# Kernel optimization log

Measured on AMD Instinct MI355X. Metric: run time of the kernel, lower is better.

Reference implementation:

```python
import jax, jax.numpy as jnp
import numpy as np

IN_DIM = 128
HID = 512


def _cell(x, h, c, Wih, Whh, bih, bhh):
    # PyTorch LSTMCell: gates = x @ Wih^T + bih + h @ Whh^T + bhh, order i,f,g,o
    g = x @ Wih.T + h @ Whh.T + (bih + bhh)
    i, f, gg, o = jnp.split(g, 4, axis=-1)
    c2 = jax.nn.sigmoid(f) * c + jax.nn.sigmoid(i) * jnp.tanh(gg)
    h2 = jax.nn.sigmoid(o) * jnp.tanh(c2)
    return h2, c2


def setup_inputs() -> dict:
    key = jax.random.key(0)
    ks = jax.random.split(key, 12)
    s1 = 1.0 / np.sqrt(HID)  # torch LSTMCell init scale
    so = 1.0 / np.sqrt(HID)
    inp = {
        "x": jax.random.normal(ks[0], (128, 1024, IN_DIM), dtype=jnp.float32),
        "Wih1": jax.random.uniform(ks[1], (4 * HID, IN_DIM), jnp.float32, -s1, s1),
        "Whh1": jax.random.uniform(ks[2], (4 * HID, HID), jnp.float32, -s1, s1),
        "bih1": jax.random.uniform(ks[3], (4 * HID,), jnp.float32, -s1, s1),
        "bhh1": jax.random.uniform(ks[4], (4 * HID,), jnp.float32, -s1, s1),
        "Wih_r": jax.random.uniform(ks[5], (4, 4 * HID, HID), jnp.float32, -s1, s1),
        "Whh_r": jax.random.uniform(ks[6], (4, 4 * HID, HID), jnp.float32, -s1, s1),
        "bih_r": jax.random.uniform(ks[7], (4, 4 * HID), jnp.float32, -s1, s1),
        "bhh_r": jax.random.uniform(ks[8], (4, 4 * HID), jnp.float32, -s1, s1),
        "Wout": jax.random.uniform(ks[9], (IN_DIM, HID), jnp.float32, -so, so),
        "bout": jax.random.uniform(ks[10], (IN_DIM,), jnp.float32, -so, so),
        "future": 0,
    }
    return inp


def reference(x, Wih1, Whh1, bih1, bhh1, Wih_r, Whh_r, bih_r, bhh_r, Wout, bout, future):
    B, T, D = x.shape
    z = jnp.zeros((B, HID), dtype=x.dtype)
    carry0 = tuple(z for _ in range(10))  # (h1,c1,...,h5,c5)

    def stack_step(carry, xt):
        h1, c1, h2, c2, h3, c3, h4, c4, h5, c5 = carry
        h1, c1 = _cell(xt, h1, c1, Wih1, Whh1, bih1, bhh1)
        h2, c2 = _cell(h1, h2, c2, Wih_r[0], Whh_r[0], bih_r[0], bhh_r[0])
        h3, c3 = _cell(h2, h3, c3, Wih_r[1], Whh_r[1], bih_r[1], bhh_r[1])
        h4, c4 = _cell(h3, h4, c4, Wih_r[2], Whh_r[2], bih_r[2], bhh_r[2])
        h5, c5 = _cell(h4, h5, c5, Wih_r[3], Whh_r[3], bih_r[3], bhh_r[3])
        return (h1, c1, h2, c2, h3, c3, h4, c4, h5, c5), h5

    carry, h5_seq = jax.lax.scan(stack_step, carry0, jnp.swapaxes(x, 0, 1))  # [T,B,H]
    outputs = jnp.einsum('tbh,dh->tbd', h5_seq, Wout) + bout  # [T,B,D]
    outputs = jnp.swapaxes(outputs, 0, 1)  # [B,T,D]

    out_t = outputs[:, -1, :]
    fut = []
    for _ in range(future):
        carry, h5 = stack_step(carry, out_t)
        out_t = h5 @ Wout.T + bout
        fut.append(out_t[:, None, :])
    if fut:
        outputs = jnp.concatenate([outputs] + fut, axis=1)
    return outputs
```

## Files before the change

kernel.cpp:

```cpp
#include <hip/hip_runtime.h>


typedef short s16x8 __attribute__((ext_vector_type(8)));
typedef float f32x4 __attribute__((ext_vector_type(4)));

#define NB   128
#define TT   1024
#define HID2 512
#define RING 16
#define RINGM 15
#define NBH  (NB * HID2)
#define STAGE_OFF (128 * 1024)

__device__ __forceinline__ unsigned short f2bf(float f) {
  union { float f; unsigned int u; } c; c.f = f;
  return (unsigned short)((c.u + 0x7fffu + ((c.u >> 16) & 1u)) >> 16);
}
__device__ __forceinline__ float sigm(float x) { return 1.0f / (1.0f + __expf(-x)); }
__device__ __forceinline__ float tanhfast(float x) {
  x = fminf(fmaxf(x, -15.0f), 15.0f);
  const float e = __expf(2.0f * x);
  return (e - 1.0f) / (e + 1.0f);
}

__global__ void convW(const float* __restrict__ Wih, const float* __restrict__ Whh,
                      const float* __restrict__ bih, const float* __restrict__ bhh,
                      unsigned short* __restrict__ Wd, float* __restrict__ biasd,
                      const int Kih, const int Khh) {
  const int K = Kih + Khh;
  const int total = 2048 * K;
  for (int idx = blockIdx.x * blockDim.x + threadIdx.x; idx < total;
       idx += gridDim.x * blockDim.x) {
    const int rp = idx / K;
    const int cc = idx - rp * K;
    const int g = rp & 3, u = rp >> 2;
    const int ro = g * 512 + u;
    const float v = (cc < Kih) ? Wih[ro * Kih + cc] : Whh[ro * Khh + (cc - Kih)];
    Wd[idx] = f2bf(v);
    if (cc == 0) biasd[rp] = bih[ro] + bhh[ro];
  }
}

__global__ void convO(const float* __restrict__ Wout, unsigned short* __restrict__ Wd) {
  for (int idx = blockIdx.x * blockDim.x + threadIdx.x; idx < 128 * 512;
       idx += gridDim.x * blockDim.x)
    Wd[idx] = f2bf(Wout[idx]);
}

#define GLD2P(D0, D1, P0, P1)                                             \
  asm volatile("global_load_dwordx4 %0, %2, off sc0 sc1\n\t"              \
               "global_load_dwordx4 %1, %3, off sc0 sc1"                  \
               : "=v"(D0), "=v"(D1) : "v"(P0), "v"(P1));
#define GLD1P(D, P)                                                       \
  asm volatile("global_load_dwordx4 %0, %1, off sc0 sc1"                  \
               : "=v"(D) : "v"(P));
#define BWAIT(D0, D1, VM)                                                 \
  asm volatile("s_waitcnt vmcnt(" VM ")" : "+v"(D0), "+v"(D1)::"memory");
#define BW1(D, VM)                                                        \
  asm volatile("s_waitcnt vmcnt(" VM ")" : "+v"(D)::"memory");

#define MFM(A, B, C) __builtin_amdgcn_mfma_f32_16x16x32_bf16(A, B, C, 0, 0, 0)
#define LDSA(MFi, AK) \
  (*reinterpret_cast<const s16x8*>(smem + (((MFi) * nkit + (AK)) << 10) + lane * 16))
#define CONSUME(SLOT, AK, VM)                                                   \
  {                                                                             \
    BWAIT(bq[SLOT][0], bq[SLOT][1], VM);                                        \
    const s16x8 af0 = LDSA(0, AK), af1 = LDSA(1, AK), af2 = LDSA(2, AK),        \
                af3 = LDSA(3, AK);                                              \
    acc[0][0] = MFM(af0, bq[SLOT][0], acc[0][0]);                               \
    acc[0][1] = MFM(af0, bq[SLOT][1], acc[0][1]);                               \
    acc[1][0] = MFM(af1, bq[SLOT][0], acc[1][0]);                               \
    acc[1][1] = MFM(af1, bq[SLOT][1], acc[1][1]);                               \
    acc[2][0] = MFM(af2, bq[SLOT][0], acc[2][0]);                               \
    acc[2][1] = MFM(af2, bq[SLOT][1], acc[2][1]);                               \
    acc[3][0] = MFM(af3, bq[SLOT][0], acc[3][0]);                               \
    acc[3][1] = MFM(af3, bq[SLOT][1], acc[3][1]);                               \
  }

#define ISSUE16K(BP)                                                            \
  GLD2P(bq[0][0], bq[0][1], (BP), (BP) + 128)                                   \
  GLD2P(bq[1][0], bq[1][1], (BP) + 4096, (BP) + 4224)                           \
  GLD2P(bq[2][0], bq[2][1], (BP) + 8192, (BP) + 8320)                           \
  GLD2P(bq[3][0], bq[3][1], (BP) + 12288, (BP) + 12416)                         \
  GLD2P(bq[4][0], bq[4][1], (BP) + 16384, (BP) + 16512)                         \
  GLD2P(bq[5][0], bq[5][1], (BP) + 20480, (BP) + 20608)                         \
  GLD2P(bq[6][0], bq[6][1], (BP) + 24576, (BP) + 24704)                         \
  GLD2P(bq[7][0], bq[7][1], (BP) + 28672, (BP) + 28800)                         \
  GLD2P(bq[8][0], bq[8][1], (BP) + 32768, (BP) + 32896)                         \
  GLD2P(bq[9][0], bq[9][1], (BP) + 36864, (BP) + 36992)                         \
  GLD2P(bq[10][0], bq[10][1], (BP) + 40960, (BP) + 41088)                       \
  GLD2P(bq[11][0], bq[11][1], (BP) + 45056, (BP) + 45184)                       \
  GLD2P(bq[12][0], bq[12][1], (BP) + 49152, (BP) + 49280)                       \
  GLD2P(bq[13][0], bq[13][1], (BP) + 53248, (BP) + 53376)                       \
  GLD2P(bq[14][0], bq[14][1], (BP) + 57344, (BP) + 57472)                       \
  GLD2P(bq[15][0], bq[15][1], (BP) + 61440, (BP) + 61568)

#define FLG(L, T) (flags + ((size_t)((L) * TT + (T)) << 5))

__global__ __launch_bounds__(256, 1) void lstm_km(
    const float* __restrict__ x,
    const unsigned short* __restrict__ W0, const unsigned short* __restrict__ W1,
    const unsigned short* __restrict__ W2, const unsigned short* __restrict__ W3,
    const unsigned short* __restrict__ W4,
    const unsigned short* __restrict__ Woutb,
    const float* __restrict__ bias,
    unsigned short* __restrict__ hring,
    unsigned int* __restrict__ flags,
    const float* __restrict__ boutp,
    float* __restrict__ outp)
{
  extern __shared__ char smem[];
  const int tid = threadIdx.x;
  const int lane = tid & 63;
  const int w = tid >> 6;
  const int l15 = lane & 15;
  const int l4 = lane >> 4;
  const int bid = blockIdx.x;

  auto pollAll = [&](const unsigned int* pa) {
    for (;;) {
      unsigned int v;
      asm volatile("global_load_dword %0, %1, off sc0 sc1\n\ts_waitcnt vmcnt(0)"
                   : "=v"(v) : "v"(pa) : "memory");
      if (__all(v != 0)) break;
      __builtin_amdgcn_s_sleep(1);
    }
  };

  if (bid < 160) {
    const int l = bid >> 5;
    const int wgi = bid & 31;
    const int K = (l == 0) ? 640 : 1024;
    const int nkit = K >> 5;
    const unsigned short* Wg = (l == 0) ? W0 : (l == 1) ? W1 : (l == 2) ? W2
                              : (l == 3) ? W3 : W4;
    const int row0 = wgi * 64;

    for (int mf = 0; mf < 4; ++mf)
      for (int kit = w; kit < nkit; kit += 4) {
        const s16x8 v = *reinterpret_cast<const s16x8*>(
            Wg + (size_t)(row0 + mf * 16 + l15) * K + kit * 32 + l4 * 8);
        *reinterpret_cast<s16x8*>(smem + ((mf * nkit + kit) << 10) + lane * 16) = v;
      }
    __syncthreads();

    float4 b4m[4];
    #pragma unroll
    for (int mf = 0; mf < 4; ++mf)
      b4m[mf] = *(const float4*)(bias + l * 2048 + row0 + mf * 16 + l4 * 4);

    float c_reg[4][2] = {};
    s16x8 bq[16][2];
    unsigned short* stage = (unsigned short*)(smem + STAGE_OFF);
    const int kcl = lane >> 5;
    const int bb = w * 32 + (lane & 31);

    for (int t = 0; t < TT; ++t) {
      const int slotP = t & RINGM, slotM = (t + RINGM) & RINGM;
      const unsigned short* hin = (l > 0)
          ? hring + (size_t)((l - 1) * RING + slotP) * NBH : nullptr;
      const unsigned short* hown = hring + (size_t)(l * RING + slotM) * NBH;
      unsigned short* hout = hring + (size_t)(l * RING + slotP) * NBH;

      f32x4 acc[4][2] = {};
      s16x8 xb[4][2];

      if (l == 0) {
        #pragma unroll
        for (int kx = 0; kx < 4; ++kx)
          #pragma unroll
          for (int nf = 0; nf < 2; ++nf) {
            const float* xs = x + ((size_t)(w * 32 + nf * 16 + l15) * TT + t) * 128
                              + kx * 32 + l4 * 8;
            const float4 v0 = *(const float4*)xs;
            const float4 v1 = *(const float4*)(xs + 4);
            union { s16x8 v; unsigned short a[8]; } pk;
            pk.a[0] = f2bf(v0.x); pk.a[1] = f2bf(v0.y); pk.a[2] = f2bf(v0.z); pk.a[3] = f2bf(v0.w);
            pk.a[4] = f2bf(v1.x); pk.a[5] = f2bf(v1.y); pk.a[6] = f2bf(v1.z); pk.a[7] = f2bf(v1.w);
            xb[kx][nf] = pk.v;
          }
      }

      if (t > 0 || l > 0) {
        const unsigned int* pa;
        if (lane < 32)
          pa = (t > 0) ? FLG(l, t - 1) + lane : FLG(l - 1, t) + lane;
        else
          pa = (l > 0) ? FLG(l - 1, t) + (lane - 32) : FLG(l, t - 1) + (lane - 32);
        pollAll(pa);
      }
      if ((t & 3) == 0 && t >= 16) {
        const unsigned int* pa = (l < 4) ? FLG(l + 1, t - 13) + (lane & 31)
                                         : FLG(5, t - 13) + (lane & 7);
        pollAll(pa);
      }

      const unsigned short* hpb = hown + ((size_t)l4 * 128 + w * 32 + l15) * 8;

      if (l == 0) {
        ISSUE16K(hpb)
        #pragma unroll
        for (int kx = 0; kx < 4; ++kx) {
          const s16x8 a0 = LDSA(0, kx), a1 = LDSA(1, kx), a2 = LDSA(2, kx), a3 = LDSA(3, kx);
          acc[0][0] = MFM(a0, xb[kx][0], acc[0][0]); acc[0][1] = MFM(a0, xb[kx][1], acc[0][1]);
          acc[1][0] = MFM(a1, xb[kx][0], acc[1][0]); acc[1][1] = MFM(a1, xb[kx][1], acc[1][1]);
          acc[2][0] = MFM(a2, xb[kx][0], acc[2][0]); acc[2][1] = MFM(a2, xb[kx][1], acc[2][1]);
          acc[3][0] = MFM(a3, xb[kx][0], acc[3][0]); acc[3][1] = MFM(a3, xb[kx][1], acc[3][1]);
        }
        CONSUME(0, 4, "30")   CONSUME(1, 5, "28")   CONSUME(2, 6, "26")   CONSUME(3, 7, "24")
        CONSUME(4, 8, "22")   CONSUME(5, 9, "20")   CONSUME(6, 10, "18")  CONSUME(7, 11, "16")
        CONSUME(8, 12, "14")  CONSUME(9, 13, "12")  CONSUME(10, 14, "10") CONSUME(11, 15, "8")
        CONSUME(12, 16, "6")  CONSUME(13, 17, "4")  CONSUME(14, 18, "2")  CONSUME(15, 19, "0")
      } else {
        const unsigned short* qpb = hin + ((size_t)l4 * 128 + w * 32 + l15) * 8;
        ISSUE16K(hpb)
        CONSUME(0, 16, "30")  GLD2P(bq[0][0], bq[0][1], qpb, qpb + 128)
        CONSUME(1, 17, "30")  GLD2P(bq[1][0], bq[1][1], qpb + 4096, qpb + 4224)
        CONSUME(2, 18, "30")  GLD2P(bq[2][0], bq[2][1], qpb + 8192, qpb + 8320)
        CONSUME(3, 19, "30")  GLD2P(bq[3][0], bq[3][1], qpb + 12288, qpb + 12416)
        CONSUME(4, 20, "30")  GLD2P(bq[4][0], bq[4][1], qpb + 16384, qpb + 16512)
        CONSUME(5, 21, "30")  GLD2P(bq[5][0], bq[5][1], qpb + 20480, qpb + 20608)
        CONSUME(6, 22, "30")  GLD2P(bq[6][0], bq[6][1], qpb + 24576, qpb + 24704)
        CONSUME(7, 23, "30")  GLD2P(bq[7][0], bq[7][1], qpb + 28672, qpb + 28800)
        CONSUME(8, 24, "30")  GLD2P(bq[8][0], bq[8][1], qpb + 32768, qpb + 32896)
        CONSUME(9, 25, "30")  GLD2P(bq[9][0], bq[9][1], qpb + 36864, qpb + 36992)
        CONSUME(10, 26, "30") GLD2P(bq[10][0], bq[10][1], qpb + 40960, qpb + 41088)
        CONSUME(11, 27, "30") GLD2P(bq[11][0], bq[11][1], qpb + 45056, qpb + 45184)
        CONSUME(12, 28, "30") GLD2P(bq[12][0], bq[12][1], qpb + 49152, qpb + 49280)
        CONSUME(13, 29, "30") GLD2P(bq[13][0], bq[13][1], qpb + 53248, qpb + 53376)
        CONSUME(14, 30, "30") GLD2P(bq[14][0], bq[14][1], qpb + 57344, qpb + 57472)
        CONSUME(15, 31, "30") GLD2P(bq[15][0], bq[15][1], qpb + 61440, qpb + 61568)
        CONSUME(0, 0, "30")   CONSUME(1, 1, "28")   CONSUME(2, 2, "26")  CONSUME(3, 3, "24")
        CONSUME(4, 4, "22")   CONSUME(5, 5, "20")   CONSUME(6, 6, "18")  CONSUME(7, 7, "16")
        CONSUME(8, 8, "14")   CONSUME(9, 9, "12")   CONSUME(10, 10, "10") CONSUME(11, 11, "8")
        CONSUME(12, 12, "6")  CONSUME(13, 13, "4")  CONSUME(14, 14, "2") CONSUME(15, 15, "0")
      }

      #pragma unroll
      for (int mf = 0; mf < 4; ++mf) {
        #pragma unroll
        for (int nf = 0; nf < 2; ++nf) {
          const float gi = acc[mf][nf][0] + b4m[mf].x;
          const float gf = acc[mf][nf][1] + b4m[mf].y;
          const float gg = acc[mf][nf][2] + b4m[mf].z;
          const float go = acc[mf][nf][3] + b4m[mf].w;
          const float cn = sigm(gf) * c_reg[mf][nf] + sigm(gi) * tanhfast(gg);
          c_reg[mf][nf] = cn;
          stage[((mf >> 1) * 128 + (w * 32 + nf * 16 + l15)) * 8 + (mf & 1) * 4 + l4] =
              f2bf(sigm(go) * tanhfast(cn));
        }
      }
      asm volatile("s_waitcnt lgkmcnt(0)" ::: "memory");
      __builtin_amdgcn_sched_barrier(0);
      {
        const s16x8 hvv = *reinterpret_cast<const s16x8*>(
            stage + ((size_t)kcl * 128 + bb) * 8);
        const unsigned short* ha = hout + ((size_t)(wgi * 2 + kcl) * 128 + bb) * 8;
        asm volatile("global_store_dwordx4 %0, %1, off sc0 sc1"
                     :: "v"(ha), "v"(hvv) : "memory");
      }
      asm volatile("s_waitcnt vmcnt(0)" ::: "memory");
      __syncthreads();
      if (tid == 0) {
        const unsigned int* fa = FLG(l, t) + wgi;
        asm volatile("global_store_dword %0, %1, off sc0 sc1" :: "v"(fa), "v"(1u) : "memory");
      }
    }
  } else {
    const int wgp = bid - 160;
    const int b0 = wgp * 16;
    for (int mf = 0; mf < 2; ++mf)
      for (int kit = 0; kit < 16; ++kit) {
        const s16x8 v = *reinterpret_cast<const s16x8*>(
            Woutb + (size_t)(w * 32 + mf * 16 + l15) * 512 + kit * 32 + l4 * 8);
        *reinterpret_cast<s16x8*>(smem + (((w * 2 + mf) * 16 + kit) << 10) + lane * 16) = v;
      }
    __syncthreads();
    float4 bo[2];
    #pragma unroll
    for (int mf = 0; mf < 2; ++mf)
      bo[mf] = *(const float4*)(boutp + w * 32 + mf * 16 + l4 * 4);

    s16x8 brp[16];
    for (int t = 0; t < TT; ++t) {
      pollAll(FLG(4, t) + (lane & 31));
      const unsigned short* h4 = hring + (size_t)(4 * RING + (t & RINGM)) * NBH;
      const unsigned short* hbK = h4 + ((size_t)l4 * 128 + b0 + l15) * 8;
      GLD1P(brp[0], hbK)           GLD1P(brp[1], hbK + 4096)
      GLD1P(brp[2], hbK + 8192)    GLD1P(brp[3], hbK + 12288)
      GLD1P(brp[4], hbK + 16384)   GLD1P(brp[5], hbK + 20480)
      GLD1P(brp[6], hbK + 24576)   GLD1P(brp[7], hbK + 28672)
      GLD1P(brp[8], hbK + 32768)   GLD1P(brp[9], hbK + 36864)
      GLD1P(brp[10], hbK + 40960)  GLD1P(brp[11], hbK + 45056)
      GLD1P(brp[12], hbK + 49152)  GLD1P(brp[13], hbK + 53248)
      GLD1P(brp[14], hbK + 57344)  GLD1P(brp[15], hbK + 61440)
      f32x4 acc2[2] = {};
      #define PCON(Q, VM)                                                        \
        {                                                                        \
          BW1(brp[Q], VM);                                                       \
          const s16x8 a0 = *reinterpret_cast<const s16x8*>(                      \
              smem + (((w * 2 + 0) * 16 + Q) << 10) + lane * 16);                \
          const s16x8 a1 = *reinterpret_cast<const s16x8*>(                      \
              smem + (((w * 2 + 1) * 16 + Q) << 10) + lane * 16);                \
          acc2[0] = MFM(a0, brp[Q], acc2[0]);                                    \
          acc2[1] = MFM(a1, brp[Q], acc2[1]);                                    \
        }
      PCON(0, "15")  PCON(1, "14")  PCON(2, "13")  PCON(3, "12")
      PCON(4, "11")  PCON(5, "10")  PCON(6, "9")   PCON(7, "8")
      PCON(8, "7")   PCON(9, "6")   PCON(10, "5")  PCON(11, "4")
      PCON(12, "3")  PCON(13, "2")  PCON(14, "1")  PCON(15, "0")
      #pragma unroll
      for (int mf = 0; mf < 2; ++mf) {
        const int d0 = w * 32 + mf * 16 + l4 * 4;
        float4 r;
        r.x = acc2[mf][0] + bo[mf].x;
        r.y = acc2[mf][1] + bo[mf].y;
        r.z = acc2[mf][2] + bo[mf].z;
        r.w = acc2[mf][3] + bo[mf].w;
        *(float4*)(outp + ((size_t)(b0 + l15) * TT + t) * 128 + d0) = r;
      }
      asm volatile("s_waitcnt vmcnt(0)" ::: "memory");
      __syncthreads();
      if (tid == 0) {
        const unsigned int* fa = FLG(5, t) + wgp;
        asm volatile("global_store_dword %0, %1, off sc0 sc1" :: "v"(fa), "v"(1u) : "memory");
      }
    }
  }
}

extern "C" void kernel_launch(void* const* d_in, const int* in_sizes, int n_in,
                              void* d_out, int out_size, void* d_ws, size_t ws_size,
                              hipStream_t stream) {
  (void)in_sizes; (void)n_in; (void)out_size; (void)ws_size;
  const float* x     = (const float*)d_in[0];
  const float* Wih1  = (const float*)d_in[1];
  const float* Whh1  = (const float*)d_in[2];
  const float* bih1  = (const float*)d_in[3];
  const float* bhh1  = (const float*)d_in[4];
  const float* Wih_r = (const float*)d_in[5];
  const float* Whh_r = (const float*)d_in[6];
  const float* bih_r = (const float*)d_in[7];
  const float* bhh_r = (const float*)d_in[8];
  const float* Wout  = (const float*)d_in[9];
  const float* boutp = (const float*)d_in[10];

  char* ws = (char*)d_ws;
  const size_t o_W0   = 0;
  const size_t o_W1   = o_W0 + 2048ull * 640 * 2;
  const size_t o_W2   = o_W1 + 2048ull * 1024 * 2;
  const size_t o_W3   = o_W2 + 2048ull * 1024 * 2;
  const size_t o_W4   = o_W3 + 2048ull * 1024 * 2;
  const size_t o_Wout = o_W4 + 2048ull * 1024 * 2;
  const size_t o_bias = o_Wout + 128ull * 512 * 2;
  const size_t o_ring = o_bias + 5ull * 2048 * 4;
  const size_t o_flag = o_ring + 5ull * RING * NBH * 2;
  const size_t o_end  = o_flag + 6ull * TT * 32 * 4;

  unsigned short* W0b  = (unsigned short*)(ws + o_W0);
  unsigned short* W1b  = (unsigned short*)(ws + o_W1);
  unsigned short* W2b  = (unsigned short*)(ws + o_W2);
  unsigned short* W3b  = (unsigned short*)(ws + o_W3);
  unsigned short* W4b  = (unsigned short*)(ws + o_W4);
  unsigned short* Wob  = (unsigned short*)(ws + o_Wout);
  float*          bias = (float*)(ws + o_bias);
  unsigned short* hrg  = (unsigned short*)(ws + o_ring);
  unsigned int*   flg  = (unsigned int*)(ws + o_flag);

  hipMemsetAsync(ws + o_ring, 0, o_end - o_ring, stream);

  convW<<<1024, 256, 0, stream>>>(Wih1, Whh1, bih1, bhh1, W0b, bias, 128, 512);
  for (int l = 1; l <= 4; ++l) {
    unsigned short* Wd = (l == 1) ? W1b : (l == 2) ? W2b : (l == 3) ? W3b : W4b;
    convW<<<1024, 256, 0, stream>>>(Wih_r + (size_t)(l - 1) * 2048 * 512,
                                    Whh_r + (size_t)(l - 1) * 2048 * 512,
                                    bih_r + (size_t)(l - 1) * 2048,
                                    bhh_r + (size_t)(l - 1) * 2048,
                                    Wd, bias + l * 2048, 512, 512);
  }
  convO<<<64, 256, 0, stream>>>(Wout, Wob);

  hipFuncSetAttribute((const void*)lstm_km,
                      hipFuncAttributeMaxDynamicSharedMemorySize, 160 * 1024);

  lstm_km<<<168, 256, 135168, stream>>>(x, W0b, W1b, W2b, W3b, W4b, Wob,
                                        bias, hrg, flg, boutp, (float*)d_out);
}
```

Measured before the change: 9.763 ms.

## Split LSTM workgroups into 8 waves with per-wave flags and direct h stores

Raises each layer workgroup from 4 to 8 waves so each wave covers 16 batch columns instead of 32, halving per-wave MFMA work and register load. It drops the LDS staging and __syncthreads before publishing h, instead storing bf16 h values straight to global and setting one completion flag per wave, with consumers polling 4-wide flag vectors. It also issues both input and recurrent h loads up front instead of interleaving them. The aim is to shorten the serial per-timestep critical path, at the cost of many small scattered short stores and more flag traffic.

```diff
diff --git a/kernel.cpp b/kernel.cpp
--- a/kernel.cpp
+++ b/kernel.cpp
@@ -3,6 +3,7 @@
 
 typedef short s16x8 __attribute__((ext_vector_type(8)));
 typedef float f32x4 __attribute__((ext_vector_type(4)));
+typedef int   i32x4 __attribute__((ext_vector_type(4)));
 
 #define NB   128
 #define TT   1024
@@ -10,7 +11,6 @@
 #define RING 16
 #define RINGM 15
 #define NBH  (NB * HID2)
-#define STAGE_OFF (128 * 1024)
 
 __device__ __forceinline__ unsigned short f2bf(float f) {
   union { float f; unsigned int u; } c; c.f = f;
@@ -47,57 +47,40 @@
     Wd[idx] = f2bf(Wout[idx]);
 }
 
-#define GLD2P(D0, D1, P0, P1)                                             \
-  asm volatile("global_load_dwordx4 %0, %2, off sc0 sc1\n\t"              \
-               "global_load_dwordx4 %1, %3, off sc0 sc1"                  \
-               : "=v"(D0), "=v"(D1) : "v"(P0), "v"(P1));
 #define GLD1P(D, P)                                                       \
   asm volatile("global_load_dwordx4 %0, %1, off sc0 sc1"                  \
                : "=v"(D) : "v"(P));
-#define BWAIT(D0, D1, VM)                                                 \
-  asm volatile("s_waitcnt vmcnt(" VM ")" : "+v"(D0), "+v"(D1)::"memory");
 #define BW1(D, VM)                                                        \
   asm volatile("s_waitcnt vmcnt(" VM ")" : "+v"(D)::"memory");
 
 #define MFM(A, B, C) __builtin_amdgcn_mfma_f32_16x16x32_bf16(A, B, C, 0, 0, 0)
 #define LDSA(MFi, AK) \
   (*reinterpret_cast<const s16x8*>(smem + (((MFi) * nkit + (AK)) << 10) + lane * 16))
-#define CONSUME(SLOT, AK, VM)                                                   \
+
+#define C8(S, AK, VM)                                                           \
   {                                                                             \
-    BWAIT(bq[SLOT][0], bq[SLOT][1], VM);                                        \
-    const s16x8 af0 = LDSA(0, AK), af1 = LDSA(1, AK), af2 = LDSA(2, AK),        \
-                af3 = LDSA(3, AK);                                              \
-    acc[0][0] = MFM(af0, bq[SLOT][0], acc[0][0]);                               \
-    acc[0][1] = MFM(af0, bq[SLOT][1], acc[0][1]);                               \
-    acc[1][0] = MFM(af1, bq[SLOT][0], acc[1][0]);                               \
-    acc[1][1] = MFM(af1, bq[SLOT][1], acc[1][1]);                               \
-    acc[2][0] = MFM(af2, bq[SLOT][0], acc[2][0]);                               \
-    acc[2][1] = MFM(af2, bq[SLOT][1], acc[2][1]);                               \
-    acc[3][0] = MFM(af3, bq[SLOT][0], acc[3][0]);                               \
-    acc[3][1] = MFM(af3, bq[SLOT][1], acc[3][1]);                               \
+    BW1(bq[S], VM);                                                             \
+    const s16x8 a0 = LDSA(0, AK), a1 = LDSA(1, AK), a2 = LDSA(2, AK),           \
+                a3 = LDSA(3, AK);                                               \
+    acc[0] = MFM(a0, bq[S], acc[0]);                                            \
+    acc[1] = MFM(a1, bq[S], acc[1]);                                            \
+    acc[2] = MFM(a2, bq[S], acc[2]);                                            \
+    acc[3] = MFM(a3, bq[S], acc[3]);                                            \
   }
 
-#define ISSUE16K(BP)                                                            \
-  GLD2P(bq[0][0], bq[0][1], (BP), (BP) + 128)                                   \
-  GLD2P(bq[1][0], bq[1][1], (BP) + 4096, (BP) + 4224)                           \
-  GLD2P(bq[2][0], bq[2][1], (BP) + 8192, (BP) + 8320)                           \
-  GLD2P(bq[3][0], bq[3][1], (BP) + 12288, (BP) + 12416)                         \
-  GLD2P(bq[4][0], bq[4][1], (BP) + 16384, (BP) + 16512)                         \
-  GLD2P(bq[5][0], bq[5][1], (BP) + 20480, (BP) + 20608)                         \
-  GLD2P(bq[6][0], bq[6][1], (BP) + 24576, (BP) + 24704)                         \
-  GLD2P(bq[7][0], bq[7][1], (BP) + 28672, (BP) + 28800)                         \
-  GLD2P(bq[8][0], bq[8][1], (BP) + 32768, (BP) + 32896)                         \
-  GLD2P(bq[9][0], bq[9][1], (BP) + 36864, (BP) + 36992)                         \
-  GLD2P(bq[10][0], bq[10][1], (BP) + 40960, (BP) + 41088)                       \
-  GLD2P(bq[11][0], bq[11][1], (BP) + 45056, (BP) + 45184)                       \
-  GLD2P(bq[12][0], bq[12][1], (BP) + 49152, (BP) + 49280)                       \
-  GLD2P(bq[13][0], bq[13][1], (BP) + 53248, (BP) + 53376)                       \
-  GLD2P(bq[14][0], bq[14][1], (BP) + 57344, (BP) + 57472)                       \
-  GLD2P(bq[15][0], bq[15][1], (BP) + 61440, (BP) + 61568)
-
-#define FLG(L, T) (flags + ((size_t)((L) * TT + (T)) << 5))
-
-__global__ __launch_bounds__(256, 1) void lstm_km(
+#define ISSUE16(BASE, P)                                                        \
+  GLD1P(bq[(BASE) + 0], (P))            GLD1P(bq[(BASE) + 1], (P) + 4096)       \
+  GLD1P(bq[(BASE) + 2], (P) + 8192)     GLD1P(bq[(BASE) + 3], (P) + 12288)      \
+  GLD1P(bq[(BASE) + 4], (P) + 16384)    GLD1P(bq[(BASE) + 5], (P) + 20480)      \
+  GLD1P(bq[(BASE) + 6], (P) + 24576)    GLD1P(bq[(BASE) + 7], (P) + 28672)      \
+  GLD1P(bq[(BASE) + 8], (P) + 32768)    GLD1P(bq[(BASE) + 9], (P) + 36864)      \
+  GLD1P(bq[(BASE) + 10], (P) + 40960)   GLD1P(bq[(BASE) + 11], (P) + 45056)     \
+  GLD1P(bq[(BASE) + 12], (P) + 49152)   GLD1P(bq[(BASE) + 13], (P) + 53248)     \
+  GLD1P(bq[(BASE) + 14], (P) + 57344)   GLD1P(bq[(BASE) + 15], (P) + 61440)
+
+#define FLG(L, T) (flags + ((size_t)((L) * TT + (T)) << 8))
+
+__global__ __launch_bounds__(512, 2) void lstm_w8(
     const float* __restrict__ x,
     const unsigned short* __restrict__ W0, const unsigned short* __restrict__ W1,
     const unsigned short* __restrict__ W2, const unsigned short* __restrict__ W3,
@@ -117,7 +100,28 @@
   const int l4 = lane >> 4;
   const int bid = blockIdx.x;
 
-  auto pollAll = [&](const unsigned int* pa) {
+  auto poll2 = [&](const unsigned int* pa, const unsigned int* pb) {
+    for (;;) {
+      i32x4 va, vb;
+      asm volatile("global_load_dwordx4 %0, %2, off sc0 sc1\n\t"
+                   "global_load_dwordx4 %1, %3, off sc0 sc1\n\t"
+                   "s_waitcnt vmcnt(0)"
+                   : "=v"(va), "=v"(vb) : "v"(pa), "v"(pb) : "memory");
+      if (__all(va[0] && va[1] && va[2] && va[3] &&
+                vb[0] && vb[1] && vb[2] && vb[3])) break;
+      __builtin_amdgcn_s_sleep(1);
+    }
+  };
+  auto poll1 = [&](const unsigned int* pa) {
+    for (;;) {
+      i32x4 va;
+      asm volatile("global_load_dwordx4 %0, %1, off sc0 sc1\n\ts_waitcnt vmcnt(0)"
+                   : "=v"(va) : "v"(pa) : "memory");
+      if (__all(va[0] && va[1] && va[2] && va[3])) break;
+      __builtin_amdgcn_s_sleep(1);
+    }
+  };
+  auto pollD = [&](const unsigned int* pa) {
     for (;;) {
       unsigned int v;
       asm volatile("global_load_dword %0, %1, off sc0 sc1\n\ts_waitcnt vmcnt(0)"
@@ -137,7 +141,7 @@
     const int row0 = wgi * 64;
 
     for (int mf = 0; mf < 4; ++mf)
-      for (int kit = w; kit < nkit; kit += 4) {
+      for (int kit = w; kit < nkit; kit += 8) {
         const s16x8 v = *reinterpret_cast<const s16x8*>(
             Wg + (size_t)(row0 + mf * 16 + l15) * K + kit * 32 + l4 * 8);
         *reinterpret_cast<s16x8*>(smem + ((mf * nkit + kit) << 10) + lane * 16) = v;
@@ -149,11 +153,8 @@
     for (int mf = 0; mf < 4; ++mf)
       b4m[mf] = *(const float4*)(bias + l * 2048 + row0 + mf * 16 + l4 * 4);
 
-    float c_reg[4][2] = {};
-    s16x8 bq[16][2];
-    unsigned short* stage = (unsigned short*)(smem + STAGE_OFF);
-    const int kcl = lane >> 5;
-    const int bb = w * 32 + (lane & 31);
+    float c_reg[4] = {0.f, 0.f, 0.f, 0.f};
+    s16x8 bq[32];
 
     for (int t = 0; t < TT; ++t) {
       const int slotP = t & RINGM, slotM = (t + RINGM) & RINGM;
@@ -162,111 +163,87 @@
       const unsigned short* hown = hring + (size_t)(l * RING + slotM) * NBH;
       unsigned short* hout = hring + (size_t)(l * RING + slotP) * NBH;
 
-      f32x4 acc[4][2] = {};
-      s16x8 xb[4][2];
+      f32x4 acc[4] = {};
+      s16x8 xb[4];
 
       if (l == 0) {
         #pragma unroll
-        for (int kx = 0; kx < 4; ++kx)
-          #pragma unroll
-          for (int nf = 0; nf < 2; ++nf) {
-            const float* xs = x + ((size_t)(w * 32 + nf * 16 + l15) * TT + t) * 128
-                              + kx * 32 + l4 * 8;
-            const float4 v0 = *(const float4*)xs;
-            const float4 v1 = *(const float4*)(xs + 4);
-            union { s16x8 v; unsigned short a[8]; } pk;
-            pk.a[0] = f2bf(v0.x); pk.a[1] = f2bf(v0.y); pk.a[2] = f2bf(v0.z); pk.a[3] = f2bf(v0.w);
-            pk.a[4] = f2bf(v1.x); pk.a[5] = f2bf(v1.y); pk.a[6] = f2bf(v1.z); pk.a[7] = f2bf(v1.w);
-            xb[kx][nf] = pk.v;
-          }
+        for (int kx = 0; kx < 4; ++kx) {
+          const float* xs = x + ((size_t)(w * 16 + l15) * TT + t) * 128
+                            + kx * 32 + l4 * 8;
+          const float4 v0 = *(const float4*)xs;
+          const float4 v1 = *(const float4*)(xs + 4);
+          union { s16x8 v; unsigned short a[8]; } pk;
+          pk.a[0] = f2bf(v0.x); pk.a[1] = f2bf(v0.y); pk.a[2] = f2bf(v0.z); pk.a[3] = f2bf(v0.w);
+          pk.a[4] = f2bf(v1.x); pk.a[5] = f2bf(v1.y); pk.a[6] = f2bf(v1.z); pk.a[7] = f2bf(v1.w);
+          xb[kx] = pk.v;
+        }
       }
 
       if (t > 0 || l > 0) {
-        const unsigned int* pa;
-        if (lane < 32)
-          pa = (t > 0) ? FLG(l, t - 1) + lane : FLG(l - 1, t) + lane;
-        else
-          pa = (l > 0) ? FLG(l - 1, t) + (lane - 32) : FLG(l, t - 1) + (lane - 32);
-        pollAll(pa);
+        const unsigned int* pa = (t > 0) ? FLG(l, t - 1) + lane * 4
+                                         : FLG(l - 1, t) + lane * 4;
+        const unsigned int* pb = (l > 0) ? FLG(l - 1, t) + lane * 4 : pa;
+        poll2(pa, pb);
       }
       if ((t & 3) == 0 && t >= 16) {
-        const unsigned int* pa = (l < 4) ? FLG(l + 1, t - 13) + (lane & 31)
-                                         : FLG(5, t - 13) + (lane & 7);
-        pollAll(pa);
-      }
-
-      const unsigned short* hpb = hown + ((size_t)l4 * 128 + w * 32 + l15) * 8;
+        if (l < 4) poll1(FLG(l + 1, t - 13) + lane * 4);
+        else       pollD(FLG(5, t - 13) + (lane & 31));
+      }
+
+      const unsigned short* ppb = hown + ((size_t)l4 * 128 + w * 16 + l15) * 8;
 
       if (l == 0) {
-        ISSUE16K(hpb)
+        ISSUE16(0, ppb)
         #pragma unroll
         for (int kx = 0; kx < 4; ++kx) {
           const s16x8 a0 = LDSA(0, kx), a1 = LDSA(1, kx), a2 = LDSA(2, kx), a3 = LDSA(3, kx);
-          acc[0][0] = MFM(a0, xb[kx][0], acc[0][0]); acc[0][1] = MFM(a0, xb[kx][1], acc[0][1]);
-          acc[1][0] = MFM(a1, xb[kx][0], acc[1][0]); acc[1][1] = MFM(a1, xb[kx][1], acc[1][1]);
-          acc[2][0] = MFM(a2, xb[kx][0], acc[2][0]); acc[2][1] = MFM(a2, xb[kx][1], acc[2][1]);
-          acc[3][0] = MFM(a3, xb[kx][0], acc[3][0]); acc[3][1] = MFM(a3, xb[kx][1], acc[3][1]);
+          acc[0] = MFM(a0, xb[kx], acc[0]);
+          acc[1] = MFM(a1, xb[kx], acc[1]);
+          acc[2] = MFM(a2, xb[kx], acc[2]);
+          acc[3] = MFM(a3, xb[kx], acc[3]);
         }
-        CONSUME(0, 4, "30")   CONSUME(1, 5, "28")   CONSUME(2, 6, "26")   CONSUME(3, 7, "24")
-        CONSUME(4, 8, "22")   CONSUME(5, 9, "20")   CONSUME(6, 10, "18")  CONSUME(7, 11, "16")
-        CONSUME(8, 12, "14")  CONSUME(9, 13, "12")  CONSUME(10, 14, "10") CONSUME(11, 15, "8")
-        CONSUME(12, 16, "6")  CONSUME(13, 17, "4")  CONSUME(14, 18, "2")  CONSUME(15, 19, "0")
+        C8(0, 4, "15")   C8(1, 5, "14")   C8(2, 6, "13")   C8(3, 7, "12")
+        C8(4, 8, "11")   C8(5, 9, "10")   C8(6, 10, "9")   C8(7, 11, "8")
+        C8(8, 12, "7")   C8(9, 13, "6")   C8(10, 14, "5")  C8(11, 15, "4")
+        C8(12, 16, "3")  C8(13, 17, "2")  C8(14, 18, "1")  C8(15, 19, "0")
       } else {
-        const unsigned short* qpb = hin + ((size_t)l4 * 128 + w * 32 + l15) * 8;
-        ISSUE16K(hpb)
-        CONSUME(0, 16, "30")  GLD2P(bq[0][0], bq[0][1], qpb, qpb + 128)
-        CONSUME(1, 17, "30")  GLD2P(bq[1][0], bq[1][1], qpb + 4096, qpb + 4224)
-        CONSUME(2, 18, "30")  GLD2P(bq[2][0], bq[2][1], qpb + 8192, qpb + 8320)
-        CONSUME(3, 19, "30")  GLD2P(bq[3][0], bq[3][1], qpb + 12288, qpb + 12416)
-        CONSUME(4, 20, "30")  GLD2P(bq[4][0], bq[4][1], qpb + 16384, qpb + 16512)
-        CONSUME(5, 21, "30")  GLD2P(bq[5][0], bq[5][1], qpb + 20480, qpb + 20608)
-        CONSUME(6, 22, "30")  GLD2P(bq[6][0], bq[6][1], qpb + 24576, qpb + 24704)
-        CONSUME(7, 23, "30")  GLD2P(bq[7][0], bq[7][1], qpb + 28672, qpb + 28800)
-        CONSUME(8, 24, "30")  GLD2P(bq[8][0], bq[8][1], qpb + 32768, qpb + 32896)
-        CONSUME(9, 25, "30")  GLD2P(bq[9][0], bq[9][1], qpb + 36864, qpb + 36992)
-        CONSUME(10, 26, "30") GLD2P(bq[10][0], bq[10][1], qpb + 40960, qpb + 41088)
-        CONSUME(11, 27, "30") GLD2P(bq[11][0], bq[11][1], qpb + 45056, qpb + 45184)
-        CONSUME(12, 28, "30") GLD2P(bq[12][0], bq[12][1], qpb + 49152, qpb + 49280)
-        CONSUME(13, 29, "30") GLD2P(bq[13][0], bq[13][1], qpb + 53248, qpb + 53376)
-        CONSUME(14, 30, "30") GLD2P(bq[14][0], bq[14][1], qpb + 57344, qpb + 57472)
-        CONSUME(15, 31, "30") GLD2P(bq[15][0], bq[15][1], qpb + 61440, qpb + 61568)
-        CONSUME(0, 0, "30")   CONSUME(1, 1, "28")   CONSUME(2, 2, "26")  CONSUME(3, 3, "24")
-        CONSUME(4, 4, "22")   CONSUME(5, 5, "20")   CONSUME(6, 6, "18")  CONSUME(7, 7, "16")
-        CONSUME(8, 8, "14")   CONSUME(9, 9, "12")   CONSUME(10, 10, "10") CONSUME(11, 11, "8")
-        CONSUME(12, 12, "6")  CONSUME(13, 13, "4")  CONSUME(14, 14, "2") CONSUME(15, 15, "0")
+        const unsigned short* qpb = hin + ((size_t)l4 * 128 + w * 16 + l15) * 8;
+        ISSUE16(0, qpb)
+        ISSUE16(16, ppb)
+        C8(0, 0, "31")   C8(1, 1, "30")   C8(2, 2, "29")   C8(3, 3, "28")
+        C8(4, 4, "27")   C8(5, 5, "26")   C8(6, 6, "25")   C8(7, 7, "24")
+        C8(8, 8, "23")   C8(9, 9, "22")   C8(10, 10, "21") C8(11, 11, "20")
+        C8(12, 12, "19") C8(13, 13, "18") C8(14, 14, "17") C8(15, 15, "16")
+        C8(16, 16, "15") C8(17, 17, "14") C8(18, 18, "13") C8(19, 19, "12")
+        C8(20, 20, "11") C8(21, 21, "10") C8(22, 22, "9")  C8(23, 23, "8")
+        C8(24, 24, "7")  C8(25, 25, "6")  C8(26, 26, "5")  C8(27, 27, "4")
+        C8(28, 28, "3")  C8(29, 29, "2")  C8(30, 30, "1")  C8(31, 31, "0")
       }
 
       #pragma unroll
       for (int mf = 0; mf < 4; ++mf) {
-        #pragma unroll
-        for (int nf = 0; nf < 2; ++nf) {
-          const float gi = acc[mf][nf][0] + b4m[mf].x;
-          const float gf = acc[mf][nf][1] + b4m[mf].y;
-          const float gg = acc[mf][nf][2] + b4m[mf].z;
-          const float go = acc[mf][nf][3] + b4m[mf].w;
-          const float cn = sigm(gf) * c_reg[mf][nf] + sigm(gi) * tanhfast(gg);
-          c_reg[mf][nf] = cn;
-          stage[((mf >> 1) * 128 + (w * 32 + nf * 16 + l15)) * 8 + (mf & 1) * 4 + l4] =
-              f2bf(sigm(go) * tanhfast(cn));
-        }
-      }
-      asm volatile("s_waitcnt lgkmcnt(0)" ::: "memory");
-      __builtin_amdgcn_sched_barrier(0);
-      {
-        const s16x8 hvv = *reinterpret_cast<const s16x8*>(
-            stage + ((size_t)kcl * 128 + bb) * 8);
-        const unsigned short* ha = hout + ((size_t)(wgi * 2 + kcl) * 128 + bb) * 8;
-        asm volatile("global_store_dwordx4 %0, %1, off sc0 sc1"
-                     :: "v"(ha), "v"(hvv) : "memory");
+        const float gi = acc[mf][0] + b4m[mf].x;
+        const float gf = acc[mf][1] + b4m[mf].y;
+        const float gg = acc[mf][2] + b4m[mf].z;
+        const float go = acc[mf][3] + b4m[mf].w;
+        const float cn = sigm(gf) * c_reg[mf] + sigm(gi) * tanhfast(gg);
+        c_reg[mf] = cn;
+        const unsigned int hv = f2bf(sigm(go) * tanhfast(cn));
+        const unsigned short* ha = hout
+            + ((size_t)(wgi * 2 + (mf >> 1)) * 128 + w * 16 + l15) * 8
+            + (mf & 1) * 4 + l4;
+        asm volatile("global_store_short %0, %1, off sc0 sc1"
+                     :: "v"(ha), "v"(hv) : "memory");
       }
       asm volatile("s_waitcnt vmcnt(0)" ::: "memory");
-      __syncthreads();
-      if (tid == 0) {
-        const unsigned int* fa = FLG(l, t) + wgi;
+      if (lane == 0) {
+        const unsigned int* fa = FLG(l, t) + wgi * 8 + w;
         asm volatile("global_store_dword %0, %1, off sc0 sc1" :: "v"(fa), "v"(1u) : "memory");
       }
     }
-  } else {
+  } else if (bid < 168) {
+    if (w >= 4) { __syncthreads(); return; }
     const int wgp = bid - 160;
     const int b0 = wgp * 16;
     for (int mf = 0; mf < 2; ++mf)
@@ -283,7 +260,7 @@
 
     s16x8 brp[16];
     for (int t = 0; t < TT; ++t) {
-      pollAll(FLG(4, t) + (lane & 31));
+      poll1(FLG(4, t) + lane * 4);
       const unsigned short* h4 = hring + (size_t)(4 * RING + (t & RINGM)) * NBH;
       const unsigned short* hbK = h4 + ((size_t)l4 * 128 + b0 + l15) * 8;
       GLD1P(brp[0], hbK)           GLD1P(brp[1], hbK + 4096)
@@ -320,9 +297,8 @@
         *(float4*)(outp + ((size_t)(b0 + l15) * TT + t) * 128 + d0) = r;
       }
       asm volatile("s_waitcnt vmcnt(0)" ::: "memory");
-      __syncthreads();
-      if (tid == 0) {
-        const unsigned int* fa = FLG(5, t) + wgp;
+      if (lane == 0) {
+        const unsigned int* fa = FLG(5, t) + wgp * 4 + w;
         asm volatile("global_store_dword %0, %1, off sc0 sc1" :: "v"(fa), "v"(1u) : "memory");
       }
     }
@@ -355,7 +331,7 @@
   const size_t o_bias = o_Wout + 128ull * 512 * 2;
   const size_t o_ring = o_bias + 5ull * 2048 * 4;
   const size_t o_flag = o_ring + 5ull * RING * NBH * 2;
-  const size_t o_end  = o_flag + 6ull * TT * 32 * 4;
+  const size_t o_end  = o_flag + 6ull * TT * 256 * 4;
 
   unsigned short* W0b  = (unsigned short*)(ws + o_W0);
   unsigned short* W1b  = (unsigned short*)(ws + o_W1);
@@ -380,9 +356,9 @@
   }
   convO<<<64, 256, 0, stream>>>(Wout, Wob);
 
-  hipFuncSetAttribute((const void*)lstm_km,
+  hipFuncSetAttribute((const void*)lstm_w8,
                       hipFuncAttributeMaxDynamicSharedMemorySize, 160 * 1024);
 
-  lstm_km<<<168, 256, 135168, stream>>>(x, W0b, W1b, W2b, W3b, W4b, Wob,
+  lstm_w8<<<168, 512, 131072, stream>>>(x, W0b, W1b, W2b, W3b, W4b, Wob,
                                         bias, hrg, flg, boutp, (float*)d_out);
 }
```

Result: slower. 11.82 ms (+21.1%).
